# Kernel tuning notes

Hardware: AMD Instinct MI355X
Metric: run time of the kernel (lower is better)

Reference implementation:

```python
import jax, jax.numpy as jnp
import numpy as np

B, S, E, H = 8, 1024, 1024, 16
D = E // H  # 64
HALF = D // 2  # 32


def _apply_rope(t, freqs):
    # t: (B, S, H, D), freqs: (S, HALF)
    emb = jnp.concatenate([freqs, freqs], axis=-1)  # (S, D)
    cos = jnp.cos(emb)[None, :, None, :]  # (1, S, 1, D)
    sin = jnp.sin(emb)[None, :, None, :]
    t1, t2 = t[..., :D // 2], t[..., D // 2:]
    rot = jnp.concatenate([-t2, t1], axis=-1)
    return t * cos + rot * sin


def setup_inputs() -> dict:
    key = jax.random.key(0)
    ks = jax.random.split(key, 10)
    std = 1.0 / np.sqrt(E)
    return {
        "hidden_states": jax.random.normal(ks[0], (B, S, E), jnp.float32),
        "rotary_pos_emb": jax.random.uniform(ks[1], (S, HALF), jnp.float32) * 10.0,
        "wq": jax.random.normal(ks[2], (E, E), jnp.float32) * std,
        "bq": jnp.zeros((E,), jnp.float32),
        "wk": jax.random.normal(ks[3], (E, E), jnp.float32) * std,
        "bk": jnp.zeros((E,), jnp.float32),
        "wv": jax.random.normal(ks[4], (E, E), jnp.float32) * std,
        "bv": jnp.zeros((E,), jnp.float32),
        "wo": jax.random.normal(ks[5], (E, E), jnp.float32) * std,
        "bo": jnp.zeros((E,), jnp.float32),
    }


def reference(hidden_states, rotary_pos_emb, wq, bq, wk, bk, wv, bv, wo, bo):
    b, s, e = hidden_states.shape
    # QKV projections -> (B, S, H, D)
    q = (hidden_states @ wq + bq).reshape(b, s, H, D)
    k = (hidden_states @ wk + bk).reshape(b, s, H, D)
    v = (hidden_states @ wv + bv).reshape(b, s, H, D)
    # rotary embedding (computed in fp32, matching the torch code)
    q = _apply_rope(q.astype(jnp.float32), rotary_pos_emb).astype(hidden_states.dtype)
    k = _apply_rope(k.astype(jnp.float32), rotary_pos_emb).astype(hidden_states.dtype)
    scale = 1.0 / np.sqrt(D)
    # attention scores (B, H, Sq, Sk)
    scores = jnp.einsum("bqhd,bkhd->bhqk", q, k) * scale
    attn = jax.nn.softmax(scores, axis=-1)
    out = jnp.einsum("bhqk,bkhd->bqhd", attn, v).reshape(b, s, e)
    return out @ wo + bo
```

## Files before the change

kernel.cpp:

```cpp
#include <hip/hip_runtime.h>
#include <hip/hip_bf16.h>

typedef __hip_bfloat16 bf16;
typedef __attribute__((ext_vector_type(8))) short bfrag;
typedef __attribute__((ext_vector_type(4))) float f32x4;

#define MFMA(a, b, c) __builtin_amdgcn_mfma_f32_16x16x32_bf16((a), (b), (c), 0, 0, 0)

__device__ __forceinline__ void async16(const void* g, void* l) {
  __builtin_amdgcn_global_load_lds(
      (const __attribute__((address_space(1))) unsigned int*)g,
      (__attribute__((address_space(3))) unsigned int*)l, 16, 0, 0);
}

__device__ __forceinline__ bfrag ldfrag(const bf16* p) { return *(const bfrag*)p; }

__device__ __forceinline__ unsigned short f2b(float f) {
  return __hip_bfloat16_raw(__float2bfloat16(f)).x;
}
__device__ __forceinline__ float b2f(short u) {
  __hip_bfloat16_raw r; r.x = (unsigned short)u;
  return __bfloat162float(__hip_bfloat16(r));
}

__device__ __forceinline__ bfrag scale8(bfrag x) {
  bfrag y;
#pragma unroll
  for (int i = 0; i < 8; i++) y[i] = (short)f2b(b2f(x[i]) * 0.125f);
  return y;
}

__device__ __forceinline__ void pack4_store(bf16* p, f32x4 v, float s) {
  union { unsigned short h[4]; uint2 u; } pk;
#pragma unroll
  for (int i = 0; i < 4; i++) pk.h[i] = f2b(v[i] * s);
  *(uint2*)p = pk.u;
}


__global__ void k_tables(const float* __restrict__ rp, float* __restrict__ ctab,
                         float* __restrict__ stab) {
  int i = blockIdx.x * 256 + threadIdx.x;
  float f = rp[i];
  ctab[i] = cosf(f);
  stab[i] = sinf(f);
}

__global__ void k_convert_x(const float* __restrict__ X, unsigned short* __restrict__ Xb) {
  int i = blockIdx.x * 256 + threadIdx.x;
  float4 v = *(const float4*)(X + (size_t)i * 4);
  union { unsigned short h[4]; uint2 u; } pk;
  pk.h[0] = f2b(v.x); pk.h[1] = f2b(v.y); pk.h[2] = f2b(v.z); pk.h[3] = f2b(v.w);
  *(uint2*)(Xb + (size_t)i * 4) = pk.u;
}

__global__ void k_transpose_w(const float* __restrict__ wq, const float* __restrict__ wk,
                              const float* __restrict__ wv, const float* __restrict__ wo,
                              unsigned short* __restrict__ tq, unsigned short* __restrict__ tk,
                              unsigned short* __restrict__ tv, unsigned short* __restrict__ to) {
  __shared__ unsigned short T[64][72];
  const int z = blockIdx.z;
  const float* src = (z == 0) ? wq : (z == 1) ? wk : (z == 2) ? wv : wo;
  unsigned short* dst = (z == 0) ? tq : (z == 1) ? tk : (z == 2) ? tv : to;
  const int k0 = blockIdx.y * 64, n0 = blockIdx.x * 64;
  const int t = threadIdx.x;
  const int kr = t >> 4;
  const int nc = (t & 15) * 4;
#pragma unroll
  for (int g = 0; g < 4; g++) {
    float4 v = *(const float4*)(src + (size_t)(k0 + g * 16 + kr) * 1024 + n0 + nc);
    const int kk = g * 16 + kr;
    T[nc + 0][kk] = f2b(v.x);
    T[nc + 1][kk] = f2b(v.y);
    T[nc + 2][kk] = f2b(v.z);
    T[nc + 3][kk] = f2b(v.w);
  }
  __syncthreads();
  const int nr = t >> 2;
  const int kc = (t & 3) * 16;
  unsigned short* dp = dst + (size_t)(n0 + nr) * 1024 + k0 + kc;
  *(uint4*)(dp + 0) = *(const uint4*)(&T[nr][kc + 0]);
  *(uint4*)(dp + 8) = *(const uint4*)(&T[nr][kc + 8]);
}


template <bool ROPE, bool F32OUT, bool BIAS_ROW, int CSTRIDE>
__device__ __forceinline__ void gemm_core(bf16* As, bf16* Bs, int m0, int n0,
                                          const bf16* __restrict__ A,
                                          const bf16* __restrict__ BT,
                                          const float* __restrict__ bias,
                                          bf16* __restrict__ C, float* __restrict__ Cf,
                                          const float* __restrict__ ctab,
                                          const float* __restrict__ stab) {
  const int tid = threadIdx.x;
  const int w = tid >> 6, l = tid & 63;
  const int wm = (w >> 1) << 6, wn = (w & 1) << 6;
  const int c = l & 15, quad = l >> 4;
  const int c7 = c & 7;

  f32x4 acc[4][4] = {};

  const int rl = l >> 3, ch = l & 7;
  const int sc = ((ch ^ rl) * 8);
  const bf16* gA = A + (size_t)(m0 + w * 32 + rl) * 1024 + sc;
  const bf16* gB = BT + (size_t)(n0 + w * 32 + rl) * 1024 + sc;
  char* lA = (char*)As + w * 32 * 128;
  char* lB = (char*)Bs + w * 32 * 128;

  for (int k0 = 0; k0 < 1024; k0 += 64) {
    __syncthreads();
#pragma unroll
    for (int g = 0; g < 4; g++) {
      async16(gA + (size_t)g * 8 * 1024 + k0, lA + g * 1024);
      async16(gB + (size_t)g * 8 * 1024 + k0, lB + g * 1024);
    }
    __syncthreads();
#pragma unroll
    for (int ks = 0; ks < 2; ks++) {
      bfrag a[4], b[4];
#pragma unroll
      for (int i = 0; i < 4; i++)
        a[i] = ldfrag(&As[(wm + i * 16 + c) * 64 + (((ks * 4 + quad) ^ c7) * 8)]);
#pragma unroll
      for (int j = 0; j < 4; j++)
        b[j] = ldfrag(&Bs[(wn + j * 16 + c) * 64 + (((ks * 4 + quad) ^ c7) * 8)]);
#pragma unroll
      for (int i = 0; i < 4; i++)
#pragma unroll
        for (int j = 0; j < 4; j++) acc[i][j] = MFMA(a[i], b[j], acc[i][j]);
    }
  }

#pragma unroll
  for (int i = 0; i < 4; i++) {
    const int mb = m0 + wm + i * 16 + quad * 4;
    if (!ROPE) {
      float brow[4];
      if (BIAS_ROW) {
#pragma unroll
        for (int r = 0; r < 4; r++) brow[r] = bias[mb + r];
      }
#pragma unroll
      for (int j = 0; j < 4; j++) {
        const int n = n0 + wn + j * 16 + c;
        const float bcol = BIAS_ROW ? 0.0f : bias[n];
#pragma unroll
        for (int r = 0; r < 4; r++) {
          const float val = acc[i][j][r] + (BIAS_ROW ? brow[r] : bcol);
          if (F32OUT)
            Cf[(size_t)(mb + r) * CSTRIDE + n] = val;
          else
            C[(size_t)(mb + r) * CSTRIDE + n] = __float2bfloat16(val);
        }
      }
    } else {
#pragma unroll
      for (int j = 0; j < 2; j++) {
        const int n1 = n0 + wn + j * 16 + c;
        const int n2 = n1 + 32;
        const int dl = j * 16 + c;
        const float b1 = bias[n1];
        const float b2 = bias[n2];
#pragma unroll
        for (int r = 0; r < 4; r++) {
          const int m = mb + r;
          const int s = m & 1023;
          const float cs = ctab[s * 32 + dl];
          const float sn = stab[s * 32 + dl];
          const float t1 = acc[i][j][r] + b1;
          const float t2 = acc[i][j + 2][r] + b2;
          C[(size_t)m * CSTRIDE + n1] = __float2bfloat16(t1 * cs - t2 * sn);
          C[(size_t)m * CSTRIDE + n2] = __float2bfloat16(t2 * cs + t1 * sn);
        }
      }
    }
  }
}

__global__ __launch_bounds__(256) void k_gemm_qkv(
    const bf16* __restrict__ X, const bf16* __restrict__ wqT, const bf16* __restrict__ wkT,
    const bf16* __restrict__ wvT, const float* __restrict__ bq, const float* __restrict__ bk,
    const float* __restrict__ bv, const float* __restrict__ ctab,
    const float* __restrict__ stab, bf16* __restrict__ Q, bf16* __restrict__ Kb,
    bf16* __restrict__ VT) {
  __shared__ __align__(16) bf16 As[128 * 64];
  __shared__ __align__(16) bf16 Bs[128 * 64];
  const int z = blockIdx.z;
  if (z == 0)
    gemm_core<true, false, false, 1024>(As, Bs, blockIdx.x * 128, blockIdx.y * 128, X, wqT,
                                        bq, Q, nullptr, ctab, stab);
  else if (z == 1)
    gemm_core<true, false, false, 1024>(As, Bs, blockIdx.x * 128, blockIdx.y * 128, X, wkT,
                                        bk, Kb, nullptr, ctab, stab);
  else
    gemm_core<false, false, true, 8192>(As, Bs, blockIdx.y * 128, blockIdx.x * 128, wvT, X,
                                        bv, VT, nullptr, nullptr, nullptr);
}

__global__ __launch_bounds__(256) void k_gemm_o(const bf16* __restrict__ A,
                                                const bf16* __restrict__ BT,
                                                const float* __restrict__ bias,
                                                float* __restrict__ Cf) {
  __shared__ __align__(16) bf16 As[128 * 64];
  __shared__ __align__(16) bf16 Bs[128 * 64];
  gemm_core<false, true, false, 1024>(As, Bs, blockIdx.x * 128, blockIdx.y * 128, A, BT,
                                      bias, nullptr, Cf, nullptr, nullptr);
}


__global__ __launch_bounds__(256, 4) void k_flash(const bf16* __restrict__ Q,
                                                  const bf16* __restrict__ K,
                                                  const bf16* __restrict__ VT,
                                                  bf16* __restrict__ O) {
  __shared__ __align__(16) bf16 Ks[64 * 64];
  __shared__ __align__(16) bf16 Vs[64 * 64];
  __shared__ __align__(16) bf16 Ps[4][32 * 72];
  const int qt = blockIdx.x, bh = blockIdx.y;
  const int b = bh >> 4, h = bh & 15;
  const int tid = threadIdx.x, w = tid >> 6, l = tid & 63;
  const int c = l & 15, quad = l >> 4;
  const int c7 = c & 7;

  bfrag qf[2][2];
#pragma unroll
  for (int qs = 0; qs < 2; qs++) {
    const bf16* qp =
        Q + (size_t)(b * 1024 + qt * 128 + w * 32 + qs * 16 + c) * 1024 + h * 64 + quad * 8;
    qf[qs][0] = scale8(ldfrag(qp));
    qf[qs][1] = scale8(ldfrag(qp + 32));
  }

  bfrag onesf;
#pragma unroll
  for (int i = 0; i < 8; i++) onesf[i] = (short)0x3F80;

  f32x4 oacc[2][4] = {};
  f32x4 lacc[2] = {};

  const int sr = l >> 3, scc = l & 7;
  const int swz = (scc ^ sr) * 8;
  const bf16* gK0 = K + (size_t)(b * 1024 + w * 16 + sr) * 1024 + h * 64 + swz;
  const bf16* gV0 = VT + (size_t)(h * 64 + w * 16 + sr) * 8192 + b * 1024 + swz;
  char* lK = (char*)Ks + w * 2048;
  char* lV = (char*)Vs + w * 2048;
  bf16* psw = Ps[w];

  for (int kt = 0; kt < 16; kt++) {
    __syncthreads();
    async16(gK0 + (size_t)(kt * 64) * 1024, lK);
    async16(gK0 + (size_t)(kt * 64 + 8) * 1024, lK + 1024);
    async16(gV0 + kt * 64, lV);
    async16(gV0 + 8 * 8192 + kt * 64, lV + 1024);
    __syncthreads();

#pragma unroll
    for (int qs = 0; qs < 2; qs++) {
      f32x4 sacc[4] = {};
#pragma unroll
      for (int mj = 0; mj < 4; mj++) {
        bfrag k0 = ldfrag(&Ks[(mj * 16 + c) * 64 + (quad ^ c7) * 8]);
        bfrag k1 = ldfrag(&Ks[(mj * 16 + c) * 64 + ((quad + 4) ^ c7) * 8]);
        sacc[mj] = MFMA(k0, qf[qs][0], sacc[mj]);
        sacc[mj] = MFMA(k1, qf[qs][1], sacc[mj]);
      }
      const int psrow = (qs * 16 + c) * 72;
#pragma unroll
      for (int mj = 0; mj < 4; mj++) {
        f32x4 p;
#pragma unroll
        for (int r = 0; r < 4; r++) p[r] = __expf(sacc[mj][r]);
        pack4_store(&psw[psrow + mj * 16 + quad * 4], p, 1.0f);
      }
    }

    bfrag pf[2][2];
#pragma unroll
    for (int qs = 0; qs < 2; qs++) {
      pf[qs][0] = ldfrag(&psw[(qs * 16 + c) * 72 + quad * 8]);
      pf[qs][1] = ldfrag(&psw[(qs * 16 + c) * 72 + 32 + quad * 8]);
      lacc[qs] = MFMA(onesf, pf[qs][0], lacc[qs]);
      lacc[qs] = MFMA(onesf, pf[qs][1], lacc[qs]);
    }
#pragma unroll
    for (int dj = 0; dj < 4; dj++) {
      bfrag v0 = ldfrag(&Vs[(dj * 16 + c) * 64 + (quad ^ c7) * 8]);
      bfrag v1 = ldfrag(&Vs[(dj * 16 + c) * 64 + ((quad + 4) ^ c7) * 8]);
#pragma unroll
      for (int qs = 0; qs < 2; qs++) {
        oacc[qs][dj] = MFMA(v0, pf[qs][0], oacc[qs][dj]);
        oacc[qs][dj] = MFMA(v1, pf[qs][1], oacc[qs][dj]);
      }
    }
  }

#pragma unroll
  for (int qs = 0; qs < 2; qs++) {
    const float inv = 1.0f / lacc[qs][0];
    bf16* op =
        O + (size_t)(b * 1024 + qt * 128 + w * 32 + qs * 16 + c) * 1024 + h * 64 + quad * 4;
#pragma unroll
    for (int dj = 0; dj < 4; dj++) pack4_store(op + dj * 16, oacc[qs][dj], inv);
  }
}


extern "C" void kernel_launch(void* const* d_in, const int* in_sizes, int n_in,
                              void* d_out, int out_size, void* d_ws, size_t ws_size,
                              hipStream_t stream) {
  const float* X  = (const float*)d_in[0];
  const float* rp = (const float*)d_in[1];
  const float* wq = (const float*)d_in[2];
  const float* bq = (const float*)d_in[3];
  const float* wk = (const float*)d_in[4];
  const float* bk = (const float*)d_in[5];
  const float* wv = (const float*)d_in[6];
  const float* bv = (const float*)d_in[7];
  const float* wo = (const float*)d_in[8];
  const float* bo = (const float*)d_in[9];
  float* out = (float*)d_out;

  char* ws = (char*)d_ws;
  const size_t MB = 1024 * 1024;
  bf16* Xb  = (bf16*)(ws + 0 * MB);
  bf16* Q   = (bf16*)(ws + 16 * MB);
  bf16* Kb  = (bf16*)(ws + 32 * MB);
  bf16* VT  = (bf16*)(ws + 48 * MB);
  bf16* O   = (bf16*)(ws + 64 * MB);
  bf16* wqT = (bf16*)(ws + 80 * MB);
  bf16* wkT = (bf16*)(ws + 82 * MB);
  bf16* wvT = (bf16*)(ws + 84 * MB);
  bf16* woT = (bf16*)(ws + 86 * MB);
  float* ctab = (float*)(ws + 88 * MB);
  float* stab = ctab + 1024 * 32;

  k_tables<<<dim3(128), dim3(256), 0, stream>>>(rp, ctab, stab);
  k_convert_x<<<dim3(8192), dim3(256), 0, stream>>>(X, (unsigned short*)Xb);
  k_transpose_w<<<dim3(16, 16, 4), dim3(256), 0, stream>>>(
      wq, wk, wv, wo, (unsigned short*)wqT, (unsigned short*)wkT, (unsigned short*)wvT,
      (unsigned short*)woT);
  k_gemm_qkv<<<dim3(64, 8, 3), dim3(256), 0, stream>>>(Xb, wqT, wkT, wvT, bq, bk, bv, ctab,
                                                       stab, Q, Kb, VT);
  k_flash<<<dim3(8, 128), dim3(256), 0, stream>>>(Q, Kb, VT, O);
  k_gemm_o<<<dim3(64, 8, 1), dim3(256), 0, stream>>>(O, woT, bo, out);
}
```

Before: 244.7 us.

## Split QKV GEMM, use 64-row tiles for V and output GEMMs, fuse table kernel

Merges the cos/sin table computation into the X conversion kernel to drop one launch. The fused QKV GEMM is split into a Q/K GEMM with RoPE that indexes contiguous wq/wk transposes via a 16-wide grid, plus a separate V^T GEMM. The V and output projections now use a 64x128 tile variant, which doubles the block count for the output GEMM to improve CU occupancy and load balance. The Q/K kernel assumes wkT sits directly after wqT in the workspace. The smaller tiles lower per-block data reuse.

```diff
diff --git a/kernel.cpp b/kernel.cpp
--- a/kernel.cpp
+++ b/kernel.cpp
@@ -38,16 +38,15 @@
 }
 
 
-__global__ void k_tables(const float* __restrict__ rp, float* __restrict__ ctab,
-                         float* __restrict__ stab) {
+__global__ void k_convert_x(const float* __restrict__ X, unsigned short* __restrict__ Xb,
+                            const float* __restrict__ rp, float* __restrict__ ctab,
+                            float* __restrict__ stab) {
   int i = blockIdx.x * 256 + threadIdx.x;
-  float f = rp[i];
-  ctab[i] = cosf(f);
-  stab[i] = sinf(f);
-}
-
-__global__ void k_convert_x(const float* __restrict__ X, unsigned short* __restrict__ Xb) {
-  int i = blockIdx.x * 256 + threadIdx.x;
+  if (blockIdx.x < 128) {
+    float f = rp[i];
+    ctab[i] = cosf(f);
+    stab[i] = sinf(f);
+  }
   float4 v = *(const float4*)(X + (size_t)i * 4);
   union { unsigned short h[4]; uint2 u; } pk;
   pk.h[0] = f2b(v.x); pk.h[1] = f2b(v.y); pk.h[2] = f2b(v.z); pk.h[3] = f2b(v.w);
@@ -84,14 +83,13 @@
 }
 
 
-template <bool ROPE, bool F32OUT, bool BIAS_ROW, int CSTRIDE>
-__device__ __forceinline__ void gemm_core(bf16* As, bf16* Bs, int m0, int n0,
-                                          const bf16* __restrict__ A,
-                                          const bf16* __restrict__ BT,
-                                          const float* __restrict__ bias,
-                                          bf16* __restrict__ C, float* __restrict__ Cf,
-                                          const float* __restrict__ ctab,
-                                          const float* __restrict__ stab) {
+__device__ __forceinline__ void gemm128_rope(bf16* As, bf16* Bs, int m0, int n0,
+                                             const bf16* __restrict__ A,
+                                             const bf16* __restrict__ BT,
+                                             const float* __restrict__ bias,
+                                             bf16* __restrict__ C,
+                                             const float* __restrict__ ctab,
+                                             const float* __restrict__ stab) {
   const int tid = threadIdx.x;
   const int w = tid >> 6, l = tid & 63;
   const int wm = (w >> 1) << 6, wn = (w & 1) << 6;
@@ -101,9 +99,9 @@
   f32x4 acc[4][4] = {};
 
   const int rl = l >> 3, ch = l & 7;
-  const int sc = ((ch ^ rl) * 8);
+  const int sc = (ch ^ rl) * 8;
   const bf16* gA = A + (size_t)(m0 + w * 32 + rl) * 1024 + sc;
-  const bf16* gB = BT + (size_t)(n0 + w * 32 + rl) * 1024 + sc;
+  const bf16* gB = BT + (size_t)(w * 32 + rl) * 1024 + sc;
   char* lA = (char*)As + w * 32 * 128;
   char* lB = (char*)Bs + w * 32 * 128;
 
@@ -134,77 +132,127 @@
 #pragma unroll
   for (int i = 0; i < 4; i++) {
     const int mb = m0 + wm + i * 16 + quad * 4;
-    if (!ROPE) {
-      float brow[4];
-      if (BIAS_ROW) {
-#pragma unroll
-        for (int r = 0; r < 4; r++) brow[r] = bias[mb + r];
-      }
-#pragma unroll
-      for (int j = 0; j < 4; j++) {
-        const int n = n0 + wn + j * 16 + c;
-        const float bcol = BIAS_ROW ? 0.0f : bias[n];
-#pragma unroll
-        for (int r = 0; r < 4; r++) {
-          const float val = acc[i][j][r] + (BIAS_ROW ? brow[r] : bcol);
-          if (F32OUT)
-            Cf[(size_t)(mb + r) * CSTRIDE + n] = val;
-          else
-            C[(size_t)(mb + r) * CSTRIDE + n] = __float2bfloat16(val);
-        }
-      }
-    } else {
-#pragma unroll
-      for (int j = 0; j < 2; j++) {
-        const int n1 = n0 + wn + j * 16 + c;
-        const int n2 = n1 + 32;
-        const int dl = j * 16 + c;
-        const float b1 = bias[n1];
-        const float b2 = bias[n2];
-#pragma unroll
-        for (int r = 0; r < 4; r++) {
-          const int m = mb + r;
-          const int s = m & 1023;
-          const float cs = ctab[s * 32 + dl];
-          const float sn = stab[s * 32 + dl];
-          const float t1 = acc[i][j][r] + b1;
-          const float t2 = acc[i][j + 2][r] + b2;
-          C[(size_t)m * CSTRIDE + n1] = __float2bfloat16(t1 * cs - t2 * sn);
-          C[(size_t)m * CSTRIDE + n2] = __float2bfloat16(t2 * cs + t1 * sn);
-        }
-      }
-    }
-  }
-}
-
-__global__ __launch_bounds__(256) void k_gemm_qkv(
-    const bf16* __restrict__ X, const bf16* __restrict__ wqT, const bf16* __restrict__ wkT,
-    const bf16* __restrict__ wvT, const float* __restrict__ bq, const float* __restrict__ bk,
-    const float* __restrict__ bv, const float* __restrict__ ctab,
-    const float* __restrict__ stab, bf16* __restrict__ Q, bf16* __restrict__ Kb,
-    bf16* __restrict__ VT) {
+#pragma unroll
+    for (int j = 0; j < 2; j++) {
+      const int n1 = n0 + wn + j * 16 + c;
+      const int n2 = n1 + 32;
+      const int dl = j * 16 + c;
+      const float b1 = bias[n1];
+      const float b2 = bias[n2];
+#pragma unroll
+      for (int r = 0; r < 4; r++) {
+        const int m = mb + r;
+        const int s = m & 1023;
+        const float cs = ctab[s * 32 + dl];
+        const float sn = stab[s * 32 + dl];
+        const float t1 = acc[i][j][r] + b1;
+        const float t2 = acc[i][j + 2][r] + b2;
+        C[(size_t)m * 1024 + n1] = __float2bfloat16(t1 * cs - t2 * sn);
+        C[(size_t)m * 1024 + n2] = __float2bfloat16(t2 * cs + t1 * sn);
+      }
+    }
+  }
+}
+
+template <bool F32OUT, bool BIAS_ROW, int CSTRIDE>
+__device__ __forceinline__ void gemm64_core(bf16* As, bf16* Bs, int m0, int n0,
+                                            const bf16* __restrict__ A,
+                                            const bf16* __restrict__ BT,
+                                            const float* __restrict__ bias,
+                                            bf16* __restrict__ C, float* __restrict__ Cf) {
+  const int tid = threadIdx.x;
+  const int w = tid >> 6, l = tid & 63;
+  const int wm = (w >> 1) << 5, wn = (w & 1) << 6;
+  const int c = l & 15, quad = l >> 4;
+  const int c7 = c & 7;
+
+  f32x4 acc[2][4] = {};
+
+  const int rl = l >> 3, ch = l & 7;
+  const int sc = (ch ^ rl) * 8;
+  const bf16* gA = A + (size_t)(m0 + w * 16 + rl) * 1024 + sc;
+  const bf16* gB = BT + (size_t)(w * 32 + rl) * 1024 + sc;
+  char* lA = (char*)As + w * 16 * 128;
+  char* lB = (char*)Bs + w * 32 * 128;
+
+  for (int k0 = 0; k0 < 1024; k0 += 64) {
+    __syncthreads();
+#pragma unroll
+    for (int g = 0; g < 2; g++) async16(gA + (size_t)g * 8 * 1024 + k0, lA + g * 1024);
+#pragma unroll
+    for (int g = 0; g < 4; g++) async16(gB + (size_t)g * 8 * 1024 + k0, lB + g * 1024);
+    __syncthreads();
+#pragma unroll
+    for (int ks = 0; ks < 2; ks++) {
+      bfrag a[2], b[4];
+#pragma unroll
+      for (int i = 0; i < 2; i++)
+        a[i] = ldfrag(&As[(wm + i * 16 + c) * 64 + (((ks * 4 + quad) ^ c7) * 8)]);
+#pragma unroll
+      for (int j = 0; j < 4; j++)
+        b[j] = ldfrag(&Bs[(wn + j * 16 + c) * 64 + (((ks * 4 + quad) ^ c7) * 8)]);
+#pragma unroll
+      for (int i = 0; i < 2; i++)
+#pragma unroll
+        for (int j = 0; j < 4; j++) acc[i][j] = MFMA(a[i], b[j], acc[i][j]);
+    }
+  }
+
+#pragma unroll
+  for (int i = 0; i < 2; i++) {
+    const int mb = m0 + wm + i * 16 + quad * 4;
+    float brow[4];
+    if (BIAS_ROW) {
+#pragma unroll
+      for (int r = 0; r < 4; r++) brow[r] = bias[mb + r];
+    }
+#pragma unroll
+    for (int j = 0; j < 4; j++) {
+      const int n = n0 + wn + j * 16 + c;
+      const float bcol = BIAS_ROW ? 0.0f : bias[n];
+#pragma unroll
+      for (int r = 0; r < 4; r++) {
+        const float val = acc[i][j][r] + (BIAS_ROW ? brow[r] : bcol);
+        if (F32OUT)
+          Cf[(size_t)(mb + r) * CSTRIDE + n] = val;
+        else
+          C[(size_t)(mb + r) * CSTRIDE + n] = __float2bfloat16(val);
+      }
+    }
+  }
+}
+
+__global__ __launch_bounds__(256) void k_gemm_qk(
+    const bf16* __restrict__ X, const bf16* __restrict__ wqkT, const float* __restrict__ bq,
+    const float* __restrict__ bk, const float* __restrict__ ctab,
+    const float* __restrict__ stab, bf16* __restrict__ Q, bf16* __restrict__ Kb) {
   __shared__ __align__(16) bf16 As[128 * 64];
   __shared__ __align__(16) bf16 Bs[128 * 64];
-  const int z = blockIdx.z;
-  if (z == 0)
-    gemm_core<true, false, false, 1024>(As, Bs, blockIdx.x * 128, blockIdx.y * 128, X, wqT,
-                                        bq, Q, nullptr, ctab, stab);
-  else if (z == 1)
-    gemm_core<true, false, false, 1024>(As, Bs, blockIdx.x * 128, blockIdx.y * 128, X, wkT,
-                                        bk, Kb, nullptr, ctab, stab);
-  else
-    gemm_core<false, false, true, 8192>(As, Bs, blockIdx.y * 128, blockIdx.x * 128, wvT, X,
-                                        bv, VT, nullptr, nullptr, nullptr);
+  const int nblk = blockIdx.y;
+  const bf16* BT = wqkT + (size_t)nblk * 128 * 1024;
+  const bool isK = nblk >= 8;
+  gemm128_rope(As, Bs, blockIdx.x * 128, (nblk & 7) * 128, X, BT, isK ? bk : bq,
+               isK ? Kb : Q, ctab, stab);
+}
+
+__global__ __launch_bounds__(256) void k_gemm_vt(const bf16* __restrict__ wvT,
+                                                 const bf16* __restrict__ X,
+                                                 const float* __restrict__ bv,
+                                                 bf16* __restrict__ VT) {
+  __shared__ __align__(16) bf16 As[64 * 64];
+  __shared__ __align__(16) bf16 Bs[128 * 64];
+  gemm64_core<false, true, 8192>(As, Bs, blockIdx.y * 64, blockIdx.x * 128, wvT,
+                                 X + (size_t)blockIdx.x * 128 * 1024, bv, VT, nullptr);
 }
 
 __global__ __launch_bounds__(256) void k_gemm_o(const bf16* __restrict__ A,
-                                                const bf16* __restrict__ BT,
+                                                const bf16* __restrict__ woT,
                                                 const float* __restrict__ bias,
                                                 float* __restrict__ Cf) {
-  __shared__ __align__(16) bf16 As[128 * 64];
+  __shared__ __align__(16) bf16 As[64 * 64];
   __shared__ __align__(16) bf16 Bs[128 * 64];
-  gemm_core<false, true, false, 1024>(As, Bs, blockIdx.x * 128, blockIdx.y * 128, A, BT,
-                                      bias, nullptr, Cf, nullptr, nullptr);
+  gemm64_core<true, false, 1024>(As, Bs, blockIdx.x * 64, blockIdx.y * 128, A,
+                                 woT + (size_t)blockIdx.y * 128 * 1024, bias, nullptr, Cf);
 }
 
 
@@ -333,13 +381,12 @@
   float* ctab = (float*)(ws + 88 * MB);
   float* stab = ctab + 1024 * 32;
 
-  k_tables<<<dim3(128), dim3(256), 0, stream>>>(rp, ctab, stab);
-  k_convert_x<<<dim3(8192), dim3(256), 0, stream>>>(X, (unsigned short*)Xb);
+  k_convert_x<<<dim3(8192), dim3(256), 0, stream>>>(X, (unsigned short*)Xb, rp, ctab, stab);
   k_transpose_w<<<dim3(16, 16, 4), dim3(256), 0, stream>>>(
       wq, wk, wv, wo, (unsigned short*)wqT, (unsigned short*)wkT, (unsigned short*)wvT,
       (unsigned short*)woT);
-  k_gemm_qkv<<<dim3(64, 8, 3), dim3(256), 0, stream>>>(Xb, wqT, wkT, wvT, bq, bk, bv, ctab,
-                                                       stab, Q, Kb, VT);
+  k_gemm_qk<<<dim3(64, 16), dim3(256), 0, stream>>>(Xb, wqT, bq, bk, ctab, stab, Q, Kb);
+  k_gemm_vt<<<dim3(64, 16), dim3(256), 0, stream>>>(wvT, Xb, bv, VT);
   k_flash<<<dim3(8, 128), dim3(256), 0, stream>>>(Q, Kb, VT, O);
-  k_gemm_o<<<dim3(64, 8, 1), dim3(256), 0, stream>>>(O, woT, bo, out);
-}
+  k_gemm_o<<<dim3(128, 8), dim3(256), 0, stream>>>(O, woT, bo, out);
+}
```

New measurement: 243.5 us. Within noise of the previous version (-0.5%).
